# Performance work log

Hardware: AMD Instinct MI355X
Metric: run time of the kernel (lower is better)

The kernel has to match this reference:

```python
import jax, jax.numpy as jnp
import numpy as np

N, E, G = 100000, 800000, 1
DV, DE, DU, H = 64, 32, 32, 128

def _w(key, shape):
    return jax.random.normal(key, shape, dtype=jnp.float32) * 0.05

def setup_inputs() -> dict:
    key = jax.random.key(0)
    ks = jax.random.split(key, 16)
    inp = {
        "node_attr": jax.random.normal(ks[0], (N, DV), dtype=jnp.float32),
        "edges": jax.random.randint(ks[1], (2, E), 0, N, dtype=jnp.int64 if jax.config.jax_enable_x64 else jnp.int32),
        "edge_attr": jax.random.normal(ks[2], (E, DE), dtype=jnp.float32),
        "u": jax.random.normal(ks[3], (G, DU), dtype=jnp.float32),
        "node_idx": jnp.zeros((N,), dtype=jnp.int32),
        "edge_idx": jnp.zeros((E,), dtype=jnp.int32),
        # edge MLP: concat(src, dst, edge_attr, u) -> H -> H
        "W1e": _w(ks[4], (2 * DV + DE + DU, H)), "b1e": jnp.zeros((H,), jnp.float32),
        "W2e": _w(ks[5], (H, H)), "b2e": jnp.zeros((H,), jnp.float32),
        # node MLP: concat(node_attr, aggregated_edges, u) -> H -> H
        "W1n": _w(ks[6], (DV + H + DU, H)), "b1n": jnp.zeros((H,), jnp.float32),
        "W2n": _w(ks[7], (H, H)), "b2n": jnp.zeros((H,), jnp.float32),
        # global MLP: concat(node_mean, edge_mean, u) -> H -> H
        "W1g": _w(ks[8], (H + H + DU, H)), "b1g": jnp.zeros((H,), jnp.float32),
        "W2g": _w(ks[9], (H, H)), "b2g": jnp.zeros((H,), jnp.float32),
    }
    return inp

def _mlp(x, W1, b1, W2, b2):
    return jax.nn.relu(x @ W1 + b1) @ W2 + b2

def _seg_mean(x, seg, num):
    s = jax.ops.segment_sum(x, seg, num_segments=num)
    c = jax.ops.segment_sum(jnp.ones((x.shape[0], 1), x.dtype), seg, num_segments=num)
    return s / jnp.maximum(c, 1.0)

def reference(node_attr, edges, edge_attr, u, node_idx, edge_idx,
              W1e, b1e, W2e, b2e, W1n, b1n, W2n, b2n, W1g, b1g, W2g, b2g):
    row, col = edges[0], edges[1]
    # edge model: gather endpoint features, concat with edge/global attrs
    e_in = jnp.concatenate([node_attr[row], node_attr[col], edge_attr, u[edge_idx]], axis=-1)
    e = _mlp(e_in, W1e, b1e, W2e, b2e)                        # [E, H]
    # node model: scatter-add incoming edge messages onto receivers (col)
    agg = jax.ops.segment_sum(e, col, num_segments=node_attr.shape[0])  # [N, H]
    v_in = jnp.concatenate([node_attr, agg, u[node_idx]], axis=-1)
    v = _mlp(v_in, W1n, b1n, W2n, b2n)                        # [N, H]
    # global model: per-graph mean pooling of nodes and edges
    nv = _seg_mean(v, node_idx, u.shape[0])                   # [G, H]
    ne = _seg_mean(e, edge_idx, u.shape[0])                   # [G, H]
    g_in = jnp.concatenate([nv, ne, u], axis=-1)
    g = _mlp(g_in, W1g, b1g, W2g, b2g)                        # [G, H]
    return v, e, g
```

## Files before the change

### kernel.cpp

```cpp
#include <hip/hip_runtime.h>

#define N_NODES 100000
#define N_EDGES 800000
#define DV 64
#define DE 32
#define DU 32
#define H 128
#define K1E 192
#define K1N 224

typedef short bf16x8 __attribute__((ext_vector_type(8)));
typedef unsigned short u16;
typedef u16 u16x8 __attribute__((ext_vector_type(8)));
typedef float f32x4 __attribute__((ext_vector_type(4)));

#define W1ET_OFF 0
#define W2ET_OFF 24576
#define W1NT_OFF 40960
#define W2NT_OFF 69632
#define WBUF_ELEMS 86016

__device__ inline u16 f2bf(float x) {
  union { float f; unsigned u; } c; c.f = x;
  unsigned r = c.u + 0x7FFFu + ((c.u >> 16) & 1u);
  return (u16)(r >> 16);
}

__global__ void prep_weights(const float* __restrict__ W1e, const float* __restrict__ W2e,
                             const float* __restrict__ W1n, const float* __restrict__ W2n,
                             u16* __restrict__ wbuf) {
  int i = blockIdx.x * blockDim.x + threadIdx.x;
  if (i < 24576) {
    int j = i / 192, k = i - j * 192;
    wbuf[W1ET_OFF + i] = f2bf(W1e[k * H + j]);
  } else if (i < 40960) {
    int t = i - 24576; int j = t >> 7, k = t & 127;
    wbuf[i] = f2bf(W2e[k * H + j]);
  } else if (i < 69632) {
    int t = i - 40960; int j = t / 224, k = t - j * 224;
    wbuf[i] = f2bf(W1n[k * H + j]);
  } else if (i < WBUF_ELEMS) {
    int t = i - 69632; int j = t >> 7, k = t & 127;
    wbuf[i] = f2bf(W2n[k * H + j]);
  }
}

__global__ __launch_bounds__(256, 2) void edge_kernel(
    const float* __restrict__ node_attr, const int* __restrict__ edges,
    const float* __restrict__ edge_attr, const float* __restrict__ uattr,
    const int* __restrict__ edge_idx, const u16* __restrict__ wbuf,
    const float* __restrict__ b1, const float* __restrict__ b2,
    float* __restrict__ e_out, float* __restrict__ agg, float* __restrict__ esum)
{
  __shared__ __align__(16) u16 X[64][200];
  __shared__ __align__(16) u16 Hs[64][136];
  __shared__ int sSrc[64], sDst[64], sEidx[64];

  const int tid = threadIdx.x;
  const int wave = tid >> 6, lane = tid & 63;
  const int l15 = lane & 15, lg = lane >> 4;
  const long e0 = (long)blockIdx.x * 64;
  const int wc = wave * 32;

  if (tid < 64)        sSrc[tid]        = edges[e0 + tid];
  else if (tid < 128)  sDst[tid - 64]   = edges[(long)N_EDGES + e0 + (tid - 64)];
  else if (tid < 192)  sEidx[tid - 128] = edge_idx[e0 + (tid - 128)];

  bf16x8 w1[6][2], w2[4][2];
  {
    const u16* w1t = wbuf + W1ET_OFF;
    const u16* w2t = wbuf + W2ET_OFF;
#pragma unroll
    for (int cf = 0; cf < 2; ++cf) {
      const u16* p1 = w1t + (wc + cf * 16 + l15) * 192 + lg * 8;
#pragma unroll
      for (int ks = 0; ks < 6; ++ks) w1[ks][cf] = *(const bf16x8*)(p1 + ks * 32);
      const u16* p2 = w2t + (wc + cf * 16 + l15) * 128 + lg * 8;
#pragma unroll
      for (int ks = 0; ks < 4; ++ks) w2[ks][cf] = *(const bf16x8*)(p2 + ks * 32);
    }
  }

  __syncthreads();

#pragma unroll
  for (int it = 0; it < 6; ++it) {
    int ch = tid + it * 256;
    int r = ch / 24, seg = ch - r * 24;
    int col = seg * 8;
    const float* src;
    if (col < 64)        src = node_attr + (long)sSrc[r] * DV + col;
    else if (col < 128)  src = node_attr + (long)sDst[r] * DV + (col - 64);
    else if (col < 160)  src = edge_attr + (e0 + r) * DE + (col - 128);
    else                 src = uattr + (long)sEidx[r] * DU + (col - 160);
    float4 f0 = *(const float4*)src;
    float4 f1 = *(const float4*)(src + 4);
    u16x8 p;
    p[0] = f2bf(f0.x); p[1] = f2bf(f0.y); p[2] = f2bf(f0.z); p[3] = f2bf(f0.w);
    p[4] = f2bf(f1.x); p[5] = f2bf(f1.y); p[6] = f2bf(f1.z); p[7] = f2bf(f1.w);
    *(u16x8*)&X[r][col] = p;
  }

  __syncthreads();

  f32x4 acc[4][2];
#pragma unroll
  for (int rf = 0; rf < 4; ++rf)
#pragma unroll
    for (int cf = 0; cf < 2; ++cf)
#pragma unroll
      for (int j = 0; j < 4; ++j) acc[rf][cf][j] = 0.f;

#pragma unroll
  for (int ks = 0; ks < 6; ++ks) {
#pragma unroll
    for (int rf = 0; rf < 4; ++rf) {
      bf16x8 a = *(const bf16x8*)&X[rf * 16 + l15][ks * 32 + lg * 8];
      acc[rf][0] = __builtin_amdgcn_mfma_f32_16x16x32_bf16(a, w1[ks][0], acc[rf][0], 0, 0, 0);
      acc[rf][1] = __builtin_amdgcn_mfma_f32_16x16x32_bf16(a, w1[ks][1], acc[rf][1], 0, 0, 0);
    }
  }

  float bias1[2] = { b1[wc + l15], b1[wc + 16 + l15] };
#pragma unroll
  for (int rf = 0; rf < 4; ++rf)
#pragma unroll
    for (int cf = 0; cf < 2; ++cf)
#pragma unroll
      for (int j = 0; j < 4; ++j) {
        float hv = acc[rf][cf][j] + bias1[cf];
        hv = hv > 0.f ? hv : 0.f;
        Hs[rf * 16 + lg * 4 + j][wc + cf * 16 + l15] = f2bf(hv);
      }

  __syncthreads();

#pragma unroll
  for (int rf = 0; rf < 4; ++rf)
#pragma unroll
    for (int cf = 0; cf < 2; ++cf)
#pragma unroll
      for (int j = 0; j < 4; ++j) acc[rf][cf][j] = 0.f;

#pragma unroll
  for (int ks = 0; ks < 4; ++ks) {
#pragma unroll
    for (int rf = 0; rf < 4; ++rf) {
      bf16x8 a = *(const bf16x8*)&Hs[rf * 16 + l15][ks * 32 + lg * 8];
      acc[rf][0] = __builtin_amdgcn_mfma_f32_16x16x32_bf16(a, w2[ks][0], acc[rf][0], 0, 0, 0);
      acc[rf][1] = __builtin_amdgcn_mfma_f32_16x16x32_bf16(a, w2[ks][1], acc[rf][1], 0, 0, 0);
    }
  }

  float bias2[2] = { b2[wc + l15], b2[wc + 16 + l15] };
  float es0 = 0.f, es1 = 0.f;
#pragma unroll
  for (int rf = 0; rf < 4; ++rf) {
#pragma unroll
    for (int cf = 0; cf < 2; ++cf) {
      int colg = wc + cf * 16 + l15;
#pragma unroll
      for (int j = 0; j < 4; ++j) {
        int r = rf * 16 + lg * 4 + j;
        float v = acc[rf][cf][j] + bias2[cf];
        e_out[(e0 + r) * H + colg] = v;
        atomicAdd(&agg[(long)sDst[r] * H + colg], v);
        if (cf == 0) es0 += v; else es1 += v;
      }
    }
  }
#pragma unroll
  for (int m = 16; m < 64; m <<= 1) { es0 += __shfl_xor(es0, m); es1 += __shfl_xor(es1, m); }
  if (lane < 16) {
    atomicAdd(&esum[wc + lane], es0);
    atomicAdd(&esum[wc + 16 + lane], es1);
  }
}

__global__ __launch_bounds__(256, 2) void node_kernel(
    const float* __restrict__ node_attr, const float* __restrict__ uattr,
    const int* __restrict__ node_idx, const u16* __restrict__ wbuf,
    const float* __restrict__ b1, const float* __restrict__ b2,
    float* __restrict__ vio, float* __restrict__ vsum)
{
  __shared__ __align__(16) u16 X[64][232];
  __shared__ __align__(16) u16 Hs[64][136];

  const int tid = threadIdx.x;
  const int wave = tid >> 6, lane = tid & 63;
  const int l15 = lane & 15, lg = lane >> 4;
  const long n0 = (long)blockIdx.x * 64;
  const int wc = wave * 32;

  bf16x8 w1[7][2], w2[4][2];
  {
    const u16* w1t = wbuf + W1NT_OFF;
    const u16* w2t = wbuf + W2NT_OFF;
#pragma unroll
    for (int cf = 0; cf < 2; ++cf) {
      const u16* p1 = w1t + (wc + cf * 16 + l15) * 224 + lg * 8;
#pragma unroll
      for (int ks = 0; ks < 7; ++ks) w1[ks][cf] = *(const bf16x8*)(p1 + ks * 32);
      const u16* p2 = w2t + (wc + cf * 16 + l15) * 128 + lg * 8;
#pragma unroll
      for (int ks = 0; ks < 4; ++ks) w2[ks][cf] = *(const bf16x8*)(p2 + ks * 32);
    }
  }

#pragma unroll
  for (int it = 0; it < 7; ++it) {
    int ch = tid + it * 256;
    int r = ch / 28, seg = ch - r * 28;
    int col = seg * 8;
    long n = n0 + r; if (n >= N_NODES) n = N_NODES - 1;
    const float* src;
    if (col < 64)        src = node_attr + n * DV + col;
    else if (col < 192)  src = vio + n * H + (col - 64);
    else                 src = uattr + (long)node_idx[n] * DU + (col - 192);
    float4 f0 = *(const float4*)src;
    float4 f1 = *(const float4*)(src + 4);
    u16x8 p;
    p[0] = f2bf(f0.x); p[1] = f2bf(f0.y); p[2] = f2bf(f0.z); p[3] = f2bf(f0.w);
    p[4] = f2bf(f1.x); p[5] = f2bf(f1.y); p[6] = f2bf(f1.z); p[7] = f2bf(f1.w);
    *(u16x8*)&X[r][col] = p;
  }

  __syncthreads();

  f32x4 acc[4][2];
#pragma unroll
  for (int rf = 0; rf < 4; ++rf)
#pragma unroll
    for (int cf = 0; cf < 2; ++cf)
#pragma unroll
      for (int j = 0; j < 4; ++j) acc[rf][cf][j] = 0.f;

#pragma unroll
  for (int ks = 0; ks < 7; ++ks) {
#pragma unroll
    for (int rf = 0; rf < 4; ++rf) {
      bf16x8 a = *(const bf16x8*)&X[rf * 16 + l15][ks * 32 + lg * 8];
      acc[rf][0] = __builtin_amdgcn_mfma_f32_16x16x32_bf16(a, w1[ks][0], acc[rf][0], 0, 0, 0);
      acc[rf][1] = __builtin_amdgcn_mfma_f32_16x16x32_bf16(a, w1[ks][1], acc[rf][1], 0, 0, 0);
    }
  }

  float bias1[2] = { b1[wc + l15], b1[wc + 16 + l15] };
#pragma unroll
  for (int rf = 0; rf < 4; ++rf)
#pragma unroll
    for (int cf = 0; cf < 2; ++cf)
#pragma unroll
      for (int j = 0; j < 4; ++j) {
        float hv = acc[rf][cf][j] + bias1[cf];
        hv = hv > 0.f ? hv : 0.f;
        Hs[rf * 16 + lg * 4 + j][wc + cf * 16 + l15] = f2bf(hv);
      }

  __syncthreads();

#pragma unroll
  for (int rf = 0; rf < 4; ++rf)
#pragma unroll
    for (int cf = 0; cf < 2; ++cf)
#pragma unroll
      for (int j = 0; j < 4; ++j) acc[rf][cf][j] = 0.f;

#pragma unroll
  for (int ks = 0; ks < 4; ++ks) {
#pragma unroll
    for (int rf = 0; rf < 4; ++rf) {
      bf16x8 a = *(const bf16x8*)&Hs[rf * 16 + l15][ks * 32 + lg * 8];
      acc[rf][0] = __builtin_amdgcn_mfma_f32_16x16x32_bf16(a, w2[ks][0], acc[rf][0], 0, 0, 0);
      acc[rf][1] = __builtin_amdgcn_mfma_f32_16x16x32_bf16(a, w2[ks][1], acc[rf][1], 0, 0, 0);
    }
  }

  float bias2[2] = { b2[wc + l15], b2[wc + 16 + l15] };
  float vs0 = 0.f, vs1 = 0.f;
#pragma unroll
  for (int rf = 0; rf < 4; ++rf) {
#pragma unroll
    for (int cf = 0; cf < 2; ++cf) {
      int colg = wc + cf * 16 + l15;
#pragma unroll
      for (int j = 0; j < 4; ++j) {
        int r = rf * 16 + lg * 4 + j;
        long n = n0 + r;
        if (n < N_NODES) {
          float v = acc[rf][cf][j] + bias2[cf];
          vio[n * H + colg] = v;
          if (cf == 0) vs0 += v; else vs1 += v;
        }
      }
    }
  }
#pragma unroll
  for (int m = 16; m < 64; m <<= 1) { vs0 += __shfl_xor(vs0, m); vs1 += __shfl_xor(vs1, m); }
  if (lane < 16) {
    atomicAdd(&vsum[wc + lane], vs0);
    atomicAdd(&vsum[wc + 16 + lane], vs1);
  }
}

__global__ void global_kernel(const float* __restrict__ uattr,
    const float* __restrict__ W1g, const float* __restrict__ b1g,
    const float* __restrict__ W2g, const float* __restrict__ b2g,
    const float* __restrict__ esum, const float* __restrict__ vsum,
    float* __restrict__ g_out)
{
  __shared__ float gin[288];
  __shared__ float hbuf[128];
  int t = threadIdx.x;
  gin[t]       = vsum[t] * (1.f / (float)N_NODES);
  gin[128 + t] = esum[t] * (1.f / (float)N_EDGES);
  if (t < 32) gin[256 + t] = uattr[t];
  __syncthreads();
  float a = b1g[t];
  for (int k = 0; k < 288; ++k) a += gin[k] * W1g[k * H + t];
  hbuf[t] = fmaxf(a, 0.f);
  __syncthreads();
  float b = b2g[t];
  for (int k = 0; k < 128; ++k) b += hbuf[k] * W2g[k * H + t];
  g_out[t] = b;
}

extern "C" void kernel_launch(void* const* d_in, const int* in_sizes, int n_in,
                              void* d_out, int out_size, void* d_ws, size_t ws_size,
                              hipStream_t stream) {
  const float* node_attr = (const float*)d_in[0];
  const int*   edges     = (const int*)d_in[1];
  const float* edge_attr = (const float*)d_in[2];
  const float* uattr     = (const float*)d_in[3];
  const int*   node_idx  = (const int*)d_in[4];
  const int*   edge_idx  = (const int*)d_in[5];
  const float* W1e = (const float*)d_in[6];  const float* b1e = (const float*)d_in[7];
  const float* W2e = (const float*)d_in[8];  const float* b2e = (const float*)d_in[9];
  const float* W1n = (const float*)d_in[10]; const float* b1n = (const float*)d_in[11];
  const float* W2n = (const float*)d_in[12]; const float* b2n = (const float*)d_in[13];
  const float* W1g = (const float*)d_in[14]; const float* b1g = (const float*)d_in[15];
  const float* W2g = (const float*)d_in[16]; const float* b2g = (const float*)d_in[17];

  float* out   = (float*)d_out;
  float* v_out = out;
  float* e_out = out + (long)N_NODES * H;
  float* g_out = out + (long)N_NODES * H + (long)N_EDGES * H;

  float* esum = (float*)d_ws;
  float* vsum = esum + 128;
  u16*   wbuf = (u16*)((char*)d_ws + 1024);

  hipMemsetAsync(v_out, 0, (size_t)N_NODES * H * sizeof(float), stream);
  hipMemsetAsync(d_ws, 0, 1024, stream);

  prep_weights<<<(WBUF_ELEMS + 255) / 256, 256, 0, stream>>>(W1e, W2e, W1n, W2n, wbuf);
  edge_kernel<<<N_EDGES / 64, 256, 0, stream>>>(node_attr, edges, edge_attr, uattr,
                                                edge_idx, wbuf, b1e, b2e,
                                                e_out, v_out, esum);
  node_kernel<<<(N_NODES + 63) / 64, 256, 0, stream>>>(node_attr, uattr, node_idx,
                                                       wbuf, b1n, b2n, v_out, vsum);
  global_kernel<<<1, 128, 0, stream>>>(uattr, W1g, b1g, W2g, b2g, esum, vsum, g_out);
}
```

Baseline: 752.4 us.

## Replace atomic scatter-add with CSR gather aggregation and stage edge output via LDS

Builds a CSR index of edges grouped by destination node (degree count, prefix scan, bucket fill), so the node kernel gathers incoming edge messages from e_out instead of the edge kernel doing 128 float atomics per edge into agg. The edge kernel now stages its output tile in shared memory and writes it with coalesced float4 stores. The global sums are spread with a stride of 16 to reduce atomic contention, and the occupancy hint rises to 3 blocks. This adds several small preprocessing kernels and a re-read of the whole e_out array in the node kernel. Summation order in the aggregation also changes.

```diff
diff --git a/kernel.cpp b/kernel.cpp
--- a/kernel.cpp
+++ b/kernel.cpp
@@ -6,19 +6,27 @@
 #define DE 32
 #define DU 32
 #define H 128
-#define K1E 192
-#define K1N 224
 
 typedef short bf16x8 __attribute__((ext_vector_type(8)));
 typedef unsigned short u16;
 typedef u16 u16x8 __attribute__((ext_vector_type(8)));
 typedef float f32x4 __attribute__((ext_vector_type(4)));
+
+#define OFF_ESUM 0
+#define OFF_VSUM 8192
+#define OFF_PART 16384
+#define OFF_WBUF 18432
+#define OFF_DEG  190464
+#define OFF_OFFS 590464
+#define OFF_BUCK 990464
 
 #define W1ET_OFF 0
 #define W2ET_OFF 24576
 #define W1NT_OFF 40960
 #define W2NT_OFF 69632
 #define WBUF_ELEMS 86016
+
+#define NPART 391
 
 __device__ inline u16 f2bf(float x) {
   union { float f; unsigned u; } c; c.f = x;
@@ -45,15 +53,75 @@
   }
 }
 
-__global__ __launch_bounds__(256, 2) void edge_kernel(
+__global__ void degree_kernel(const int* __restrict__ edges, int* __restrict__ deg) {
+  int i = blockIdx.x * 256 + threadIdx.x;
+  if (i < N_EDGES) atomicAdd(&deg[edges[N_EDGES + i]], 1);
+}
+
+__global__ void scan_part(const int* __restrict__ deg, int* __restrict__ part) {
+  int i = blockIdx.x * 256 + threadIdx.x;
+  int v = (i < N_NODES) ? deg[i] : 0;
+#pragma unroll
+  for (int m = 1; m < 64; m <<= 1) v += __shfl_xor(v, m);
+  __shared__ int s[4];
+  if ((threadIdx.x & 63) == 0) s[threadIdx.x >> 6] = v;
+  __syncthreads();
+  if (threadIdx.x == 0) part[blockIdx.x] = s[0] + s[1] + s[2] + s[3];
+}
+
+__global__ void scan_top(int* __restrict__ part) {
+  __shared__ int s[512];
+  int t = threadIdx.x;
+  s[t] = (t < NPART) ? part[t] : 0;
+  __syncthreads();
+  for (int d = 1; d < 512; d <<= 1) {
+    int v = (t >= d) ? s[t - d] : 0;
+    __syncthreads();
+    s[t] += v;
+    __syncthreads();
+  }
+  if (t < NPART) part[t] = (t == 0) ? 0 : s[t - 1];
+}
+
+__global__ void scan_down(const int* __restrict__ part, int* __restrict__ deg_cursor,
+                          int* __restrict__ offsets) {
+  __shared__ int s[256];
+  int b = blockIdx.x, t = threadIdx.x;
+  int i = b * 256 + t;
+  int v = (i < N_NODES) ? deg_cursor[i] : 0;
+  s[t] = v;
+  __syncthreads();
+  for (int d = 1; d < 256; d <<= 1) {
+    int u = (t >= d) ? s[t - d] : 0;
+    __syncthreads();
+    s[t] += u;
+    __syncthreads();
+  }
+  int excl = s[t] - v + part[b];
+  if (i < N_NODES) { offsets[i] = excl; deg_cursor[i] = excl; }
+}
+
+__global__ void fill_kernel(const int* __restrict__ edges, int* __restrict__ cursor,
+                            int* __restrict__ bucket) {
+  int i = blockIdx.x * 256 + threadIdx.x;
+  if (i < N_EDGES) {
+    int d = edges[N_EDGES + i];
+    int pos = atomicAdd(&cursor[d], 1);
+    bucket[pos] = i;
+  }
+}
+
+__global__ __launch_bounds__(256, 3) void edge_kernel(
     const float* __restrict__ node_attr, const int* __restrict__ edges,
     const float* __restrict__ edge_attr, const float* __restrict__ uattr,
     const int* __restrict__ edge_idx, const u16* __restrict__ wbuf,
     const float* __restrict__ b1, const float* __restrict__ b2,
-    float* __restrict__ e_out, float* __restrict__ agg, float* __restrict__ esum)
+    float* __restrict__ e_out, float* __restrict__ esum_p)
 {
-  __shared__ __align__(16) u16 X[64][200];
-  __shared__ __align__(16) u16 Hs[64][136];
+  __shared__ __align__(16) char smem[43008];
+  u16 (*X)[200]   = (u16(*)[200])smem;
+  u16 (*Hs)[136]  = (u16(*)[136])(smem + 25600);
+  float (*OT)[132] = (float(*)[132])smem;
   __shared__ int sSrc[64], sDst[64], sEidx[64];
 
   const int tid = threadIdx.x;
@@ -152,36 +220,48 @@
     }
   }
 
+  __syncthreads();
+
   float bias2[2] = { b2[wc + l15], b2[wc + 16 + l15] };
   float es0 = 0.f, es1 = 0.f;
 #pragma unroll
   for (int rf = 0; rf < 4; ++rf) {
 #pragma unroll
     for (int cf = 0; cf < 2; ++cf) {
-      int colg = wc + cf * 16 + l15;
 #pragma unroll
       for (int j = 0; j < 4; ++j) {
-        int r = rf * 16 + lg * 4 + j;
         float v = acc[rf][cf][j] + bias2[cf];
-        e_out[(e0 + r) * H + colg] = v;
-        atomicAdd(&agg[(long)sDst[r] * H + colg], v);
+        OT[rf * 16 + lg * 4 + j][wc + cf * 16 + l15] = v;
         if (cf == 0) es0 += v; else es1 += v;
       }
     }
   }
+
+  __syncthreads();
+
+#pragma unroll
+  for (int i = 0; i < 8; ++i) {
+    int ch = tid + i * 256;
+    int r = ch >> 5, c4 = ch & 31;
+    float4 f = *(const float4*)&OT[r][c4 * 4];
+    *(float4*)(e_out + (e0 + r) * H + c4 * 4) = f;
+  }
+
 #pragma unroll
   for (int m = 16; m < 64; m <<= 1) { es0 += __shfl_xor(es0, m); es1 += __shfl_xor(es1, m); }
   if (lane < 16) {
-    atomicAdd(&esum[wc + lane], es0);
-    atomicAdd(&esum[wc + 16 + lane], es1);
-  }
-}
-
-__global__ __launch_bounds__(256, 2) void node_kernel(
+    atomicAdd(&esum_p[(wc + lane) * 16], es0);
+    atomicAdd(&esum_p[(wc + 16 + lane) * 16], es1);
+  }
+}
+
+__global__ __launch_bounds__(256, 3) void node_kernel(
     const float* __restrict__ node_attr, const float* __restrict__ uattr,
     const int* __restrict__ node_idx, const u16* __restrict__ wbuf,
     const float* __restrict__ b1, const float* __restrict__ b2,
-    float* __restrict__ vio, float* __restrict__ vsum)
+    const float* __restrict__ e_out, const int* __restrict__ offsets,
+    const int* __restrict__ cursor, const int* __restrict__ bucket,
+    float* __restrict__ v_out, float* __restrict__ vsum_p)
 {
   __shared__ __align__(16) u16 X[64][232];
   __shared__ __align__(16) u16 Hs[64][136];
@@ -192,31 +272,43 @@
   const long n0 = (long)blockIdx.x * 64;
   const int wc = wave * 32;
 
-  bf16x8 w1[7][2], w2[4][2];
   {
-    const u16* w1t = wbuf + W1NT_OFF;
-    const u16* w2t = wbuf + W2NT_OFF;
-#pragma unroll
-    for (int cf = 0; cf < 2; ++cf) {
-      const u16* p1 = w1t + (wc + cf * 16 + l15) * 224 + lg * 8;
-#pragma unroll
-      for (int ks = 0; ks < 7; ++ks) w1[ks][cf] = *(const bf16x8*)(p1 + ks * 32);
-      const u16* p2 = w2t + (wc + cf * 16 + l15) * 128 + lg * 8;
-#pragma unroll
-      for (int ks = 0; ks < 4; ++ks) w2[ks][cf] = *(const bf16x8*)(p2 + ks * 32);
-    }
-  }
-
-#pragma unroll
-  for (int it = 0; it < 7; ++it) {
+    int gr = tid >> 2, gq = tid & 3;
+    long gn = n0 + gr;
+    float a[32];
+#pragma unroll
+    for (int k = 0; k < 32; ++k) a[k] = 0.f;
+    if (gn < N_NODES) {
+      int s = offsets[gn], e = cursor[gn];
+      for (int i = s; i < e; ++i) {
+        int eid = bucket[i];
+        const float* p = e_out + (long)eid * H + gq * 32;
+#pragma unroll
+        for (int k = 0; k < 8; ++k) {
+          float4 f = *(const float4*)(p + k * 4);
+          a[k * 4 + 0] += f.x; a[k * 4 + 1] += f.y;
+          a[k * 4 + 2] += f.z; a[k * 4 + 3] += f.w;
+        }
+      }
+    }
+#pragma unroll
+    for (int k = 0; k < 4; ++k) {
+      u16x8 pk;
+#pragma unroll
+      for (int j = 0; j < 8; ++j) pk[j] = f2bf(a[k * 8 + j]);
+      *(u16x8*)&X[gr][64 + gq * 32 + k * 8] = pk;
+    }
+  }
+
+#pragma unroll
+  for (int it = 0; it < 3; ++it) {
     int ch = tid + it * 256;
-    int r = ch / 28, seg = ch - r * 28;
-    int col = seg * 8;
+    int r = ch / 12, seg = ch - r * 12;
     long n = n0 + r; if (n >= N_NODES) n = N_NODES - 1;
     const float* src;
-    if (col < 64)        src = node_attr + n * DV + col;
-    else if (col < 192)  src = vio + n * H + (col - 64);
-    else                 src = uattr + (long)node_idx[n] * DU + (col - 192);
+    int col;
+    if (seg < 8) { col = seg * 8;            src = node_attr + n * DV + col; }
+    else         { col = 192 + (seg - 8) * 8; src = uattr + (long)node_idx[n] * DU + (seg - 8) * 8; }
     float4 f0 = *(const float4*)src;
     float4 f1 = *(const float4*)(src + 4);
     u16x8 p;
@@ -225,6 +317,21 @@
     *(u16x8*)&X[r][col] = p;
   }
 
+  bf16x8 w1[7][2], w2[4][2];
+  {
+    const u16* w1t = wbuf + W1NT_OFF;
+    const u16* w2t = wbuf + W2NT_OFF;
+#pragma unroll
+    for (int cf = 0; cf < 2; ++cf) {
+      const u16* p1 = w1t + (wc + cf * 16 + l15) * 224 + lg * 8;
+#pragma unroll
+      for (int ks = 0; ks < 7; ++ks) w1[ks][cf] = *(const bf16x8*)(p1 + ks * 32);
+      const u16* p2 = w2t + (wc + cf * 16 + l15) * 128 + lg * 8;
+#pragma unroll
+      for (int ks = 0; ks < 4; ++ks) w2[ks][cf] = *(const bf16x8*)(p2 + ks * 32);
+    }
+  }
+
   __syncthreads();
 
   f32x4 acc[4][2];
@@ -289,7 +396,7 @@
         long n = n0 + r;
         if (n < N_NODES) {
           float v = acc[rf][cf][j] + bias2[cf];
-          vio[n * H + colg] = v;
+          v_out[n * H + colg] = v;
           if (cf == 0) vs0 += v; else vs1 += v;
         }
       }
@@ -298,22 +405,22 @@
 #pragma unroll
   for (int m = 16; m < 64; m <<= 1) { vs0 += __shfl_xor(vs0, m); vs1 += __shfl_xor(vs1, m); }
   if (lane < 16) {
-    atomicAdd(&vsum[wc + lane], vs0);
-    atomicAdd(&vsum[wc + 16 + lane], vs1);
+    atomicAdd(&vsum_p[(wc + lane) * 16], vs0);
+    atomicAdd(&vsum_p[(wc + 16 + lane) * 16], vs1);
   }
 }
 
 __global__ void global_kernel(const float* __restrict__ uattr,
     const float* __restrict__ W1g, const float* __restrict__ b1g,
     const float* __restrict__ W2g, const float* __restrict__ b2g,
-    const float* __restrict__ esum, const float* __restrict__ vsum,
+    const float* __restrict__ esum_p, const float* __restrict__ vsum_p,
     float* __restrict__ g_out)
 {
   __shared__ float gin[288];
   __shared__ float hbuf[128];
   int t = threadIdx.x;
-  gin[t]       = vsum[t] * (1.f / (float)N_NODES);
-  gin[128 + t] = esum[t] * (1.f / (float)N_EDGES);
+  gin[t]       = vsum_p[t * 16] * (1.f / (float)N_NODES);
+  gin[128 + t] = esum_p[t * 16] * (1.f / (float)N_EDGES);
   if (t < 32) gin[256 + t] = uattr[t];
   __syncthreads();
   float a = b1g[t];
@@ -346,18 +453,31 @@
   float* e_out = out + (long)N_NODES * H;
   float* g_out = out + (long)N_NODES * H + (long)N_EDGES * H;
 
-  float* esum = (float*)d_ws;
-  float* vsum = esum + 128;
-  u16*   wbuf = (u16*)((char*)d_ws + 1024);
-
-  hipMemsetAsync(v_out, 0, (size_t)N_NODES * H * sizeof(float), stream);
-  hipMemsetAsync(d_ws, 0, 1024, stream);
-
-  prep_weights<<<(WBUF_ELEMS + 255) / 256, 256, 0, stream>>>(W1e, W2e, W1n, W2n, wbuf);
+  char* ws = (char*)d_ws;
+  float* esum_p = (float*)(ws + OFF_ESUM);
+  float* vsum_p = (float*)(ws + OFF_VSUM);
+  int*   part   = (int*)(ws + OFF_PART);
+  u16*   wbuf   = (u16*)(ws + OFF_WBUF);
+  int*   deg    = (int*)(ws + OFF_DEG);
+  int*   offs   = (int*)(ws + OFF_OFFS);
+  int*   buck   = (int*)(ws + OFF_BUCK);
+
+  hipMemsetAsync(ws, 0, 16384, stream);
+  hipMemsetAsync(deg, 0, N_NODES * sizeof(int), stream);
+
+  prep_weights<<<WBUF_ELEMS / 256, 256, 0, stream>>>(W1e, W2e, W1n, W2n, wbuf);
+  degree_kernel<<<(N_EDGES + 255) / 256, 256, 0, stream>>>(edges, deg);
+  scan_part<<<NPART, 256, 0, stream>>>(deg, part);
+  scan_top<<<1, 512, 0, stream>>>(part);
+  scan_down<<<NPART, 256, 0, stream>>>(part, deg, offs);
+  fill_kernel<<<(N_EDGES + 255) / 256, 256, 0, stream>>>(edges, deg, buck);
+
   edge_kernel<<<N_EDGES / 64, 256, 0, stream>>>(node_attr, edges, edge_attr, uattr,
                                                 edge_idx, wbuf, b1e, b2e,
-                                                e_out, v_out, esum);
+                                                e_out, esum_p);
   node_kernel<<<(N_NODES + 63) / 64, 256, 0, stream>>>(node_attr, uattr, node_idx,
-                                                       wbuf, b1n, b2n, v_out, vsum);
-  global_kernel<<<1, 128, 0, stream>>>(uattr, W1g, b1g, W2g, b2g, esum, vsum, g_out);
-}
+                                                       wbuf, b1n, b2n,
+                                                       e_out, offs, deg, buck,
+                                                       v_out, vsum_p);
+  global_kernel<<<1, 128, 0, stream>>>(uattr, W1g, b1g, W2g, b2g, esum_p, vsum_p, g_out);
+}
```

Result: faster. 619.5 us (-17.7%).
